# Performance work log

Measured on AMD Instinct MI355X. Metric: run time of the kernel, lower is better.

Reference implementation:

```python
import jax, jax.numpy as jnp
import numpy as np

B, E, F_DIM, D = 32, 16, 64, 512  # batch, extra dim, fea_dim, input_dim
EXP = 4                            # feed-forward expansion
EPS = 1e-5


def _layernorm(x, g, b):
    m = jnp.mean(x, axis=-1, keepdims=True)
    v = jnp.mean(jnp.square(x - m), axis=-1, keepdims=True)
    return (x - m) * jax.lax.rsqrt(v + EPS) * g + b


def setup_inputs() -> dict:
    key = jax.random.key(0)
    ks = jax.random.split(key, 12)
    s = 1.0 / np.sqrt(D)
    inp = {
        "x": jax.random.normal(ks[0], (B, E, F_DIM, D), jnp.float32),
        "ln1_g": jnp.ones((D,), jnp.float32),
        "ln1_b": jnp.zeros((D,), jnp.float32),
        "Wq": jax.random.uniform(ks[1], (D, D), jnp.float32, -s, s),
        "bq": jax.random.uniform(ks[2], (D,), jnp.float32, -s, s),
        "Wk": jax.random.uniform(ks[3], (D, D), jnp.float32, -s, s),
        "bk": jax.random.uniform(ks[4], (D,), jnp.float32, -s, s),
        "Wv": jax.random.uniform(ks[5], (D, D), jnp.float32, -s, s),
        "bv": jax.random.uniform(ks[6], (D,), jnp.float32, -s, s),
        "wn_g": jnp.ones((F_DIM,), jnp.float32),
        "wn_b": jnp.zeros((F_DIM,), jnp.float32),
        "ln2_g": jnp.ones((D,), jnp.float32),
        "ln2_b": jnp.zeros((D,), jnp.float32),
        "W1": jax.random.uniform(ks[7], (D, EXP * D), jnp.float32, -s, s),
        "b1": jax.random.uniform(ks[8], (EXP * D,), jnp.float32, -s, s),
        "W2": jax.random.uniform(ks[9], (EXP * D, D), jnp.float32, -1.0 / np.sqrt(EXP * D), 1.0 / np.sqrt(EXP * D)),
        "b2": jax.random.uniform(ks[10], (D,), jnp.float32, -1.0 / np.sqrt(EXP * D), 1.0 / np.sqrt(EXP * D)),
    }
    return inp


def reference(x, ln1_g, ln1_b, Wq, bq, Wk, bk, Wv, bv, wn_g, wn_b, ln2_g, ln2_b, W1, b1, W2, b2):
    # --- Residual 1: LN -> feature multi-head attention (dropout = identity) ---
    h = _layernorm(x, ln1_g, ln1_b)                       # [B,E,F,D]
    q = h @ Wq + bq
    k = h @ Wk + bk
    v = h @ Wv + bv
    energy = jnp.einsum('beqd,bekd->beqk', q, k)          # [B,E,F,F]
    # LayerNorm over the key axis of the raw scores (the fusion-breaking op)
    energy = _layernorm(energy, wn_g, wn_b)
    att = jax.nn.softmax(energy / jnp.sqrt(jnp.float32(D)), axis=-1)
    attn_out = jnp.einsum('beal,belv->beav', att, v)      # [B,E,F,D]
    x = x + attn_out
    # --- Residual 2: LN -> FFN (Linear -> Linear, no activation) ---
    h2 = _layernorm(x, ln2_g, ln2_b)
    ff = (h2 @ W1 + b1) @ W2 + b2
    return x + ff
```

## Files before the change

### kernel.cpp

```cpp
#include <hip/hip_runtime.h>
#include <hip/hip_bf16.h>


#define D_DIM 512
#define NROWS 32768
#define NBE   512

typedef __attribute__((ext_vector_type(8))) short bf16x8;
typedef __attribute__((ext_vector_type(4))) float f32x4;

typedef const __attribute__((address_space(1))) unsigned g_u32;
typedef __attribute__((address_space(3))) unsigned lds_u32;

__device__ __forceinline__ short f2bf(float f) {
  union { float f; unsigned u; } c; c.f = f;
  unsigned u = c.u;
  unsigned r = (u + 0x7FFFu + ((u >> 16) & 1u)) >> 16;
  return (short)r;
}
__device__ __forceinline__ float bf2f(short s) {
  union { unsigned u; float f; } c; c.u = ((unsigned)(unsigned short)s) << 16;
  return c.f;
}

__global__ __launch_bounds__(256) void wconvT(const float* __restrict__ W,
                                              short* __restrict__ Wt,
                                              int K, int N) {
  __shared__ float tile[32][33];
  const int t = threadIdx.x;
  const int r  = t >> 3;
  const int c4 = (t & 7) * 4;
  const long k0 = (long)blockIdx.y * 32;
  const long n0 = (long)blockIdx.x * 32;
  float4 v = *(const float4*)&W[(k0 + r) * N + n0 + c4];
  tile[r][c4 + 0] = v.x; tile[r][c4 + 1] = v.y;
  tile[r][c4 + 2] = v.z; tile[r][c4 + 3] = v.w;
  __syncthreads();
  union { short sh[4]; int2 v; } o;
#pragma unroll
  for (int j = 0; j < 4; ++j) o.sh[j] = f2bf(tile[c4 + j][r]);
  *(int2*)&Wt[(n0 + r) * K + k0 + c4] = o.v;
}

__global__ __launch_bounds__(256) void ln_kernel(const float* __restrict__ x,
                                                 const float* __restrict__ gam,
                                                 const float* __restrict__ bet,
                                                 short* __restrict__ h) {
  const int t = threadIdx.x;
  const long row = (long)blockIdx.x * 4 + (t >> 6);
  const int lane = t & 63;
  const float* xr = x + row * D_DIM + lane * 8;
  float4 a = *(const float4*)xr;
  float4 b = *(const float4*)(xr + 4);
  float xs[8] = {a.x, a.y, a.z, a.w, b.x, b.y, b.z, b.w};
  float s = 0.f, ss = 0.f;
#pragma unroll
  for (int j = 0; j < 8; ++j) { s += xs[j]; ss += xs[j] * xs[j]; }
#pragma unroll
  for (int m = 1; m < 64; m <<= 1) {
    s  += __shfl_xor(s, m);
    ss += __shfl_xor(ss, m);
  }
  float mean = s * (1.f / D_DIM);
  float var  = ss * (1.f / D_DIM) - mean * mean;
  float rstd = rsqrtf(var + 1e-5f);
  union { short sh[8]; int4 v; } o;
#pragma unroll
  for (int j = 0; j < 8; ++j) {
    int d = lane * 8 + j;
    o.sh[j] = f2bf((xs[j] - mean) * rstd * gam[d] + bet[d]);
  }
  *(int4*)&h[row * D_DIM + lane * 8] = o.v;
}

template <int OUT_BF16, int RESID>
__global__ __launch_bounds__(512, 2) void gemm256(
    const short* __restrict__ A, const short* __restrict__ Bt,
    const float* __restrict__ bias0, const float* __restrict__ bias1,
    const float* __restrict__ bias2,
    void* __restrict__ out0, void* __restrict__ out1, void* __restrict__ out2,
    const float* __restrict__ resid, int K, int nsplit) {
  extern __shared__ short smem[];
  short* As = smem;
  short* Bs = smem + 3 * 8192;

  const int t = threadIdx.x;
  const int wave = t >> 6, lane = t & 63;
  const int lr = lane & 15, g = lane >> 4;
  const int wr = wave >> 2, wc = wave & 3;

  const int gx = gridDim.x;
  const int nwg = gx * gridDim.y;
  const int hid = blockIdx.y * gx + blockIdx.x;
  const int lid = (hid & 7) * (nwg >> 3) + (hid >> 3);
  const int m0 = (lid / gx) * 256;
  const int n0 = (lid % gx) * 256;

  const int seg = n0 / nsplit;
  const int ncol0 = n0 - seg * nsplit;
  const float* bias = seg == 0 ? bias0 : (seg == 1 ? bias1 : bias2);
  void* outp = seg == 0 ? out0 : (seg == 1 ? out1 : out2);

  const int srow = lane & 15;
  const int scol = (lane >> 4) * 8;
  const short* gA0 = &A[(long)(m0 + wave * 32 + srow) * K + scol];
  const short* gB0 = &Bt[(long)(n0 + wave * 32 + srow) * K + scol];
  const long rstep = 16L * K;

#define STAGE_A(bufi, kk)                                                      \
  do {                                                                         \
    __builtin_amdgcn_global_load_lds((g_u32*)(gA0 + (kk)),                     \
        (lds_u32*)(As + (bufi) * 8192 + (wave * 2) * 512), 16, 0, 0);          \
    __builtin_amdgcn_global_load_lds((g_u32*)(gA0 + rstep + (kk)),             \
        (lds_u32*)(As + (bufi) * 8192 + (wave * 2 + 1) * 512), 16, 0, 0);      \
  } while (0)
#define STAGE_B(bufi, kk)                                                      \
  do {                                                                         \
    __builtin_amdgcn_global_load_lds((g_u32*)(gB0 + (kk)),                     \
        (lds_u32*)(Bs + (bufi) * 8192 + (wave * 2) * 512), 16, 0, 0);          \
    __builtin_amdgcn_global_load_lds((g_u32*)(gB0 + rstep + (kk)),             \
        (lds_u32*)(Bs + (bufi) * 8192 + (wave * 2 + 1) * 512), 16, 0, 0);      \
  } while (0)

  f32x4 acc[8][4];
  const f32x4 vzero = {0.f, 0.f, 0.f, 0.f};
#pragma unroll
  for (int mi = 0; mi < 8; ++mi)
#pragma unroll
    for (int ni = 0; ni < 4; ++ni) acc[mi][ni] = vzero;

  const int nt = K >> 5;
  STAGE_A(0, 0);  STAGE_B(0, 0);
  STAGE_A(1, 32); STAGE_B(1, 32);

  int cur = 0, stg = 2;
  const int fo = lane * 8;
  for (int T = 0; T < nt; ++T) {
    if (T < nt - 1) asm volatile("s_waitcnt vmcnt(4)" ::: "memory");
    else            asm volatile("s_waitcnt vmcnt(0)" ::: "memory");
    asm volatile("s_barrier" ::: "memory");

    if (T + 2 < nt) {
      STAGE_A(stg, (T + 2) * 32);
      STAGE_B(stg, (T + 2) * 32);
    }

    const short* sA = As + cur * 8192;
    const short* sB = Bs + cur * 8192;
    bf16x8 af[8], bfr[4];
#pragma unroll
    for (int i = 0; i < 8; ++i)
      af[i] = *(const bf16x8*)&sA[(wr * 8 + i) * 512 + fo];
#pragma unroll
    for (int i = 0; i < 4; ++i)
      bfr[i] = *(const bf16x8*)&sB[(wc * 4 + i) * 512 + fo];
#pragma unroll
    for (int mi = 0; mi < 8; ++mi)
#pragma unroll
      for (int ni = 0; ni < 4; ++ni)
        acc[mi][ni] = __builtin_amdgcn_mfma_f32_16x16x32_bf16(af[mi], bfr[ni], acc[mi][ni], 0, 0, 0);

    cur = cur == 2 ? 0 : cur + 1;
    stg = stg == 2 ? 0 : stg + 1;
  }
#undef STAGE_A
#undef STAGE_B

  __syncthreads();
  float* cs = (float*)smem + wave * 1088;
  float bv[4];
#pragma unroll
  for (int ni = 0; ni < 4; ++ni) bv[ni] = bias[ncol0 + wc * 64 + ni * 16 + lr];
  const int er = lane >> 2;
  const int ec = (lane & 3) * 16;

#pragma unroll
  for (int mi = 0; mi < 8; ++mi) {
#pragma unroll
    for (int ni = 0; ni < 4; ++ni)
#pragma unroll
      for (int r = 0; r < 4; ++r)
        cs[(g * 4 + r) * 68 + ni * 16 + lr] = acc[mi][ni][r] + bv[ni];
    const long grow = m0 + wr * 128 + mi * 16 + er;
    const long gcol = ncol0 + wc * 64 + ec;
    float vals[16];
#pragma unroll
    for (int jb = 0; jb < 4; ++jb) {
      float4 v = *(const float4*)&cs[er * 68 + ec + jb * 4];
      vals[jb * 4 + 0] = v.x; vals[jb * 4 + 1] = v.y;
      vals[jb * 4 + 2] = v.z; vals[jb * 4 + 3] = v.w;
    }
    if (RESID) {
      const float* rp = resid + grow * (long)nsplit + gcol;
#pragma unroll
      for (int jb = 0; jb < 4; ++jb) {
        float4 v = *(const float4*)&rp[jb * 4];
        vals[jb * 4 + 0] += v.x; vals[jb * 4 + 1] += v.y;
        vals[jb * 4 + 2] += v.z; vals[jb * 4 + 3] += v.w;
      }
    }
    if (OUT_BF16) {
      union { short sh[16]; int4 q[2]; } o;
#pragma unroll
      for (int j = 0; j < 16; ++j) o.sh[j] = f2bf(vals[j]);
      short* op = (short*)outp + grow * (long)nsplit + gcol;
      *(int4*)op = o.q[0];
      *(int4*)(op + 8) = o.q[1];
    } else {
      float* op = (float*)outp + grow * (long)nsplit + gcol;
#pragma unroll
      for (int jb = 0; jb < 4; ++jb)
        *(float4*)&op[jb * 4] = make_float4(vals[jb * 4 + 0], vals[jb * 4 + 1],
                                            vals[jb * 4 + 2], vals[jb * 4 + 3]);
    }
  }
}

__global__ __launch_bounds__(256) void attn_kernel(
    const short* __restrict__ q, const short* __restrict__ k,
    const short* __restrict__ v, const float* __restrict__ x,
    const float* __restrict__ wn_g, const float* __restrict__ wn_b,
    const float* __restrict__ ln2_g, const float* __restrict__ ln2_b,
    float* __restrict__ x1, short* __restrict__ h2) {
  __shared__ float att_s[64][68];
  const int t = threadIdx.x;
  const int wave = t >> 6, lane = t & 63;
  const int lr = lane & 15, g = lane >> 4;
  const long base = (long)blockIdx.x * 64;
  const long qoff = base * D_DIM;

  const f32x4 vzero = {0.f, 0.f, 0.f, 0.f};
  f32x4 acc[4];
#pragma unroll
  for (int nt = 0; nt < 4; ++nt) acc[nt] = vzero;

  for (int ks = 0; ks < 16; ++ks) {
    const int kc = ks * 32 + g * 8;
    bf16x8 afr = *(const bf16x8*)&q[qoff + (long)(wave * 16 + lr) * D_DIM + kc];
#pragma unroll
    for (int nt = 0; nt < 4; ++nt) {
      bf16x8 bfr = *(const bf16x8*)&k[qoff + (long)(nt * 16 + lr) * D_DIM + kc];
      acc[nt] = __builtin_amdgcn_mfma_f32_16x16x32_bf16(afr, bfr, acc[nt], 0, 0, 0);
    }
  }

  const float scale = 0.044194173824159216f;
#pragma unroll
  for (int r = 0; r < 4; ++r) {
    float s = 0.f, ss = 0.f;
#pragma unroll
    for (int nt = 0; nt < 4; ++nt) { float e = acc[nt][r]; s += e; ss += e * e; }
#pragma unroll
    for (int m = 1; m < 16; m <<= 1) { s += __shfl_xor(s, m); ss += __shfl_xor(ss, m); }
    float mean = s * (1.f / 64);
    float var  = ss * (1.f / 64) - mean * mean;
    float rstd = rsqrtf(var + 1e-5f);
    float e[4]; float mx = -1e30f;
#pragma unroll
    for (int nt = 0; nt < 4; ++nt) {
      int col = nt * 16 + lr;
      e[nt] = ((acc[nt][r] - mean) * rstd * wn_g[col] + wn_b[col]) * scale;
      mx = fmaxf(mx, e[nt]);
    }
#pragma unroll
    for (int m = 1; m < 16; m <<= 1) mx = fmaxf(mx, __shfl_xor(mx, m));
    float se = 0.f;
#pragma unroll
    for (int nt = 0; nt < 4; ++nt) { e[nt] = expf(e[nt] - mx); se += e[nt]; }
#pragma unroll
    for (int m = 1; m < 16; m <<= 1) se += __shfl_xor(se, m);
    float inv = 1.f / se;
#pragma unroll
    for (int nt = 0; nt < 4; ++nt)
      att_s[wave * 16 + 4 * g + r][nt * 16 + lr] = e[nt] * inv;
  }
  __syncthreads();

  const int d0 = lane * 8;
  float accp[16][8];
#pragma unroll
  for (int qi = 0; qi < 16; ++qi)
#pragma unroll
    for (int j = 0; j < 8; ++j) accp[qi][j] = 0.f;

  for (int kk0 = 0; kk0 < 64; kk0 += 4) {
    float vf[4][8];
#pragma unroll
    for (int kc = 0; kc < 4; ++kc) {
      bf16x8 vv = *(const bf16x8*)&v[qoff + (long)(kk0 + kc) * D_DIM + d0];
#pragma unroll
      for (int j = 0; j < 8; ++j) vf[kc][j] = bf2f(vv[j]);
    }
#pragma unroll
    for (int qi = 0; qi < 16; ++qi) {
      float4 a4 = *(const float4*)&att_s[wave * 16 + qi][kk0];
#pragma unroll
      for (int j = 0; j < 8; ++j) {
        accp[qi][j] += a4.x * vf[0][j];
        accp[qi][j] += a4.y * vf[1][j];
        accp[qi][j] += a4.z * vf[2][j];
        accp[qi][j] += a4.w * vf[3][j];
      }
    }
  }

  float g2v[8], b2v[8];
#pragma unroll
  for (int j = 0; j < 8; ++j) { g2v[j] = ln2_g[d0 + j]; b2v[j] = ln2_b[d0 + j]; }

#pragma unroll
  for (int qi = 0; qi < 16; ++qi) {
    const long row = base + wave * 16 + qi;
    const float* xr = x + row * D_DIM + d0;
    float4 x0 = *(const float4*)xr;
    float4 xb = *(const float4*)(xr + 4);
    accp[qi][0] += x0.x; accp[qi][1] += x0.y;
    accp[qi][2] += x0.z; accp[qi][3] += x0.w;
    accp[qi][4] += xb.x; accp[qi][5] += xb.y;
    accp[qi][6] += xb.z; accp[qi][7] += xb.w;
    float* po = x1 + row * D_DIM + d0;
    *(float4*)po       = make_float4(accp[qi][0], accp[qi][1], accp[qi][2], accp[qi][3]);
    *(float4*)(po + 4) = make_float4(accp[qi][4], accp[qi][5], accp[qi][6], accp[qi][7]);
    float s = 0.f, ss = 0.f;
#pragma unroll
    for (int j = 0; j < 8; ++j) { s += accp[qi][j]; ss += accp[qi][j] * accp[qi][j]; }
#pragma unroll
    for (int m = 1; m < 64; m <<= 1) { s += __shfl_xor(s, m); ss += __shfl_xor(ss, m); }
    float mean = s * (1.f / D_DIM);
    float var  = ss * (1.f / D_DIM) - mean * mean;
    float rstd = rsqrtf(var + 1e-5f);
    union { short sh[8]; int4 v; } o;
#pragma unroll
    for (int j = 0; j < 8; ++j)
      o.sh[j] = f2bf((accp[qi][j] - mean) * rstd * g2v[j] + b2v[j]);
    *(int4*)&h2[row * D_DIM + d0] = o.v;
  }
}

extern "C" void kernel_launch(void* const* d_in, const int* in_sizes, int n_in,
                              void* d_out, int out_size, void* d_ws, size_t ws_size,
                              hipStream_t stream) {
  (void)in_sizes; (void)n_in; (void)out_size; (void)ws_size;
  const float* x     = (const float*)d_in[0];
  const float* ln1_g = (const float*)d_in[1];
  const float* ln1_b = (const float*)d_in[2];
  const float* Wq    = (const float*)d_in[3];
  const float* bq    = (const float*)d_in[4];
  const float* Wk    = (const float*)d_in[5];
  const float* bk    = (const float*)d_in[6];
  const float* Wv    = (const float*)d_in[7];
  const float* bv    = (const float*)d_in[8];
  const float* wn_g  = (const float*)d_in[9];
  const float* wn_b  = (const float*)d_in[10];
  const float* ln2_g = (const float*)d_in[11];
  const float* ln2_b = (const float*)d_in[12];
  const float* W1    = (const float*)d_in[13];
  const float* b1    = (const float*)d_in[14];
  const float* W2    = (const float*)d_in[15];
  const float* b2    = (const float*)d_in[16];
  float* out = (float*)d_out;

  char* ws = (char*)d_ws;
  short* h   = (short*)(ws);
  short* qb  = (short*)(ws + (size_t)32  * 1024 * 1024);
  short* kb  = (short*)(ws + (size_t)64  * 1024 * 1024);
  short* vb  = (short*)(ws + (size_t)96  * 1024 * 1024);
  short* ff1 = (short*)(ws + (size_t)32  * 1024 * 1024);
  short* Wqt = (short*)(ws + (size_t)160 * 1024 * 1024);
  short* Wkt = Wqt + 512 * 512;
  short* Wvt = Wkt + 512 * 512;
  short* W1t = Wvt + 512 * 512;
  short* W2t = W1t + 512 * 2048;

  const size_t lds_bytes = 3 * 8192 * 2 * 2;
  (void)hipFuncSetAttribute((const void*)gemm256<1, 0>,
      hipFuncAttributeMaxDynamicSharedMemorySize, (int)lds_bytes);
  (void)hipFuncSetAttribute((const void*)gemm256<0, 1>,
      hipFuncAttributeMaxDynamicSharedMemorySize, (int)lds_bytes);

  wconvT<<<dim3(512 / 32, 512 / 32),  256, 0, stream>>>(Wq, Wqt, 512, 512);
  wconvT<<<dim3(512 / 32, 512 / 32),  256, 0, stream>>>(Wk, Wkt, 512, 512);
  wconvT<<<dim3(512 / 32, 512 / 32),  256, 0, stream>>>(Wv, Wvt, 512, 512);
  wconvT<<<dim3(2048 / 32, 512 / 32), 256, 0, stream>>>(W1, W1t, 512, 2048);
  wconvT<<<dim3(512 / 32, 2048 / 32), 256, 0, stream>>>(W2, W2t, 2048, 512);

  ln_kernel<<<NROWS / 4, 256, 0, stream>>>(x, ln1_g, ln1_b, h);

  dim3 gqkv(1536 / 256, NROWS / 256);
  gemm256<1, 0><<<gqkv, 512, lds_bytes, stream>>>(h, Wqt, bq, bk, bv,
                                                  qb, kb, vb, nullptr, 512, 512);

  attn_kernel<<<NBE, 256, 0, stream>>>(qb, kb, vb, x, wn_g, wn_b,
                                       ln2_g, ln2_b, out, h);

  dim3 gff1(2048 / 256, NROWS / 256);
  gemm256<1, 0><<<gff1, 512, lds_bytes, stream>>>(h, W1t, b1, b1, b1,
                                                  ff1, ff1, ff1, nullptr, 512, 2048);

  dim3 gff2(512 / 256, NROWS / 256);
  gemm256<0, 1><<<gff2, 512, lds_bytes, stream>>>(ff1, W2t, b2, b2, b2,
                                                  out, out, out, out, 2048, 512);
}
```

Measured before the change: 507.8 us.

## Restructure GEMM to double-buffered BK=64 with XOR-swizzled row-major LDS tiles

The 256x256 GEMM's K-step grows from 32 to 64 and staging moves from a triple-buffered, fragment-ordered LDS layout to a double-buffered row-major layout with an XOR swizzle that avoids bank conflicts. Each iteration now issues 16 MFMAs per fragment set across two K halves and uses a __syncthreads per step, replacing the manual vmcnt waits and s_barrier. LDS rises to 128 KB and the min-blocks-per-CU hint of 2 is removed, which halves barriers per unit of K but lowers occupancy. Prefetch depth drops from two stages ahead to one.

```diff
diff --git a/kernel.cpp b/kernel.cpp
--- a/kernel.cpp
+++ b/kernel.cpp
@@ -74,7 +74,7 @@
 }
 
 template <int OUT_BF16, int RESID>
-__global__ __launch_bounds__(512, 2) void gemm256(
+__global__ __launch_bounds__(512) void gemm256(
     const short* __restrict__ A, const short* __restrict__ Bt,
     const float* __restrict__ bias0, const float* __restrict__ bias1,
     const float* __restrict__ bias2,
@@ -82,7 +82,7 @@
     const float* __restrict__ resid, int K, int nsplit) {
   extern __shared__ short smem[];
   short* As = smem;
-  short* Bs = smem + 3 * 8192;
+  short* Bs = smem + 2 * 16384;
 
   const int t = threadIdx.x;
   const int wave = t >> 6, lane = t & 63;
@@ -101,25 +101,23 @@
   const float* bias = seg == 0 ? bias0 : (seg == 1 ? bias1 : bias2);
   void* outp = seg == 0 ? out0 : (seg == 1 ? out1 : out2);
 
-  const int srow = lane & 15;
-  const int scol = (lane >> 4) * 8;
-  const short* gA0 = &A[(long)(m0 + wave * 32 + srow) * K + scol];
-  const short* gB0 = &Bt[(long)(n0 + wave * 32 + srow) * K + scol];
-  const long rstep = 16L * K;
-
-#define STAGE_A(bufi, kk)                                                      \
+  const int srow = lane >> 3;
+  const int skel = 8 * ((lane & 7) ^ srow);
+  const short* gA0 = &A[(long)(m0 + wave * 32 + srow) * K + skel];
+  const short* gB0 = &Bt[(long)(n0 + wave * 32 + srow) * K + skel];
+  const long rstep8 = 8L * K;
+
+#define STAGE(bufi, kk)                                                        \
   do {                                                                         \
-    __builtin_amdgcn_global_load_lds((g_u32*)(gA0 + (kk)),                     \
-        (lds_u32*)(As + (bufi) * 8192 + (wave * 2) * 512), 16, 0, 0);          \
-    __builtin_amdgcn_global_load_lds((g_u32*)(gA0 + rstep + (kk)),             \
-        (lds_u32*)(As + (bufi) * 8192 + (wave * 2 + 1) * 512), 16, 0, 0);      \
-  } while (0)
-#define STAGE_B(bufi, kk)                                                      \
-  do {                                                                         \
-    __builtin_amdgcn_global_load_lds((g_u32*)(gB0 + (kk)),                     \
-        (lds_u32*)(Bs + (bufi) * 8192 + (wave * 2) * 512), 16, 0, 0);          \
-    __builtin_amdgcn_global_load_lds((g_u32*)(gB0 + rstep + (kk)),             \
-        (lds_u32*)(Bs + (bufi) * 8192 + (wave * 2 + 1) * 512), 16, 0, 0);      \
+    _Pragma("unroll")                                                          \
+    for (int i = 0; i < 4; ++i) {                                              \
+      __builtin_amdgcn_global_load_lds((g_u32*)(gA0 + i * rstep8 + (kk)),      \
+          (lds_u32*)(As + (bufi) * 16384 + wave * 2048 + i * 512 + lane * 8),  \
+          16, 0, 0);                                                           \
+      __builtin_amdgcn_global_load_lds((g_u32*)(gB0 + i * rstep8 + (kk)),      \
+          (lds_u32*)(Bs + (bufi) * 16384 + wave * 2048 + i * 512 + lane * 8),  \
+          16, 0, 0);                                                           \
+    }                                                                          \
   } while (0)
 
   f32x4 acc[8][4];
@@ -129,44 +127,44 @@
 #pragma unroll
     for (int ni = 0; ni < 4; ++ni) acc[mi][ni] = vzero;
 
-  const int nt = K >> 5;
-  STAGE_A(0, 0);  STAGE_B(0, 0);
-  STAGE_A(1, 32); STAGE_B(1, 32);
-
-  int cur = 0, stg = 2;
-  const int fo = lane * 8;
+  const int nt = K >> 6;
+  STAGE(0, 0);
+  __syncthreads();
+
+  const int fswz = (lr & 7) * 8;
+  int cur = 0;
   for (int T = 0; T < nt; ++T) {
-    if (T < nt - 1) asm volatile("s_waitcnt vmcnt(4)" ::: "memory");
-    else            asm volatile("s_waitcnt vmcnt(0)" ::: "memory");
-    asm volatile("s_barrier" ::: "memory");
-
-    if (T + 2 < nt) {
-      STAGE_A(stg, (T + 2) * 32);
-      STAGE_B(stg, (T + 2) * 32);
-    }
-
-    const short* sA = As + cur * 8192;
-    const short* sB = Bs + cur * 8192;
-    bf16x8 af[8], bfr[4];
-#pragma unroll
-    for (int i = 0; i < 8; ++i)
-      af[i] = *(const bf16x8*)&sA[(wr * 8 + i) * 512 + fo];
-#pragma unroll
-    for (int i = 0; i < 4; ++i)
-      bfr[i] = *(const bf16x8*)&sB[(wc * 4 + i) * 512 + fo];
-#pragma unroll
-    for (int mi = 0; mi < 8; ++mi)
-#pragma unroll
-      for (int ni = 0; ni < 4; ++ni)
-        acc[mi][ni] = __builtin_amdgcn_mfma_f32_16x16x32_bf16(af[mi], bfr[ni], acc[mi][ni], 0, 0, 0);
-
-    cur = cur == 2 ? 0 : cur + 1;
-    stg = stg == 2 ? 0 : stg + 1;
-  }
-#undef STAGE_A
-#undef STAGE_B
-
-  __syncthreads();
+    if (T + 1 < nt) STAGE(cur ^ 1, (T + 1) * 64);
+    const short* sA = As + cur * 16384;
+    const short* sB = Bs + cur * 16384;
+    bf16x8 af[8][2], bfr[4][2];
+#pragma unroll
+    for (int c = 0; c < 8; ++c) {
+      const int rbase = (wr * 128 + c * 16 + lr) * 64;
+#pragma unroll
+      for (int t2 = 0; t2 < 2; ++t2)
+        af[c][t2] = *(const bf16x8*)&sA[rbase + ((t2 * 32 + g * 8) ^ fswz)];
+    }
+#pragma unroll
+    for (int c = 0; c < 4; ++c) {
+      const int rbase = (wc * 64 + c * 16 + lr) * 64;
+#pragma unroll
+      for (int t2 = 0; t2 < 2; ++t2)
+        bfr[c][t2] = *(const bf16x8*)&sB[rbase + ((t2 * 32 + g * 8) ^ fswz)];
+    }
+#pragma unroll
+    for (int t2 = 0; t2 < 2; ++t2)
+#pragma unroll
+      for (int mi = 0; mi < 8; ++mi)
+#pragma unroll
+        for (int ni = 0; ni < 4; ++ni)
+          acc[mi][ni] = __builtin_amdgcn_mfma_f32_16x16x32_bf16(
+              af[mi][t2], bfr[ni][t2], acc[mi][ni], 0, 0, 0);
+    __syncthreads();
+    cur ^= 1;
+  }
+#undef STAGE
+
   float* cs = (float*)smem + wave * 1088;
   float bv[4];
 #pragma unroll
@@ -372,7 +370,7 @@
   short* W1t = Wvt + 512 * 512;
   short* W2t = W1t + 512 * 2048;
 
-  const size_t lds_bytes = 3 * 8192 * 2 * 2;
+  const size_t lds_bytes = 4 * 16384 * 2;
   (void)hipFuncSetAttribute((const void*)gemm256<1, 0>,
       hipFuncAttributeMaxDynamicSharedMemorySize, (int)lds_bytes);
   (void)hipFuncSetAttribute((const void*)gemm256<0, 1>,
```

Result: faster. 496.4 us (-2.3%).

## Restructure GEMM main loop into 4-phase ping-pong schedule with 64-wide K tiles

Applied to the files above, without the earlier changes.

Rewrites the gemm256 main loop to use 64-wide K tiles split into two 32-wide halves, double-buffered in 128 KB of LDS. Each iteration runs four phases, each loading a fragment set, issuing one quarter of the next tiles' global-to-LDS loads, and then doing MFMAs at raised wave priority between barriers. The aim is to interleave memory traffic with matrix work and reduce stall time at barriers. In exchange the larger LDS footprint drops occupancy to one workgroup per CU (launch bounds changed to match), and the schedule adds many more barriers.

```diff
diff --git a/kernel.cpp b/kernel.cpp
--- a/kernel.cpp
+++ b/kernel.cpp
@@ -74,16 +74,13 @@
 }
 
 template <int OUT_BF16, int RESID>
-__global__ __launch_bounds__(512, 2) void gemm256(
+__global__ __launch_bounds__(512) void gemm256(
     const short* __restrict__ A, const short* __restrict__ Bt,
     const float* __restrict__ bias0, const float* __restrict__ bias1,
     const float* __restrict__ bias2,
     void* __restrict__ out0, void* __restrict__ out1, void* __restrict__ out2,
     const float* __restrict__ resid, int K, int nsplit) {
   extern __shared__ short smem[];
-  short* As = smem;
-  short* Bs = smem + 3 * 8192;
-
   const int t = threadIdx.x;
   const int wave = t >> 6, lane = t & 63;
   const int lr = lane & 15, g = lane >> 4;
@@ -101,25 +98,27 @@
   const float* bias = seg == 0 ? bias0 : (seg == 1 ? bias1 : bias2);
   void* outp = seg == 0 ? out0 : (seg == 1 ? out1 : out2);
 
-  const int srow = lane & 15;
-  const int scol = (lane >> 4) * 8;
-  const short* gA0 = &A[(long)(m0 + wave * 32 + srow) * K + scol];
-  const short* gB0 = &Bt[(long)(n0 + wave * 32 + srow) * K + scol];
-  const long rstep = 16L * K;
-
-#define STAGE_A(bufi, kk)                                                      \
+  const short* gA0 = &A[(long)(m0 + wave * 16 + lr) * K + g * 8];
+  const short* gB0 = &Bt[(long)(n0 + wave * 16 + lr) * K + g * 8];
+  const long rstep = 128L * K;
+  const int ldst = wave * 512 + lane * 8;
+
+#define STG_A(bb, kh, Ti)                                                      \
   do {                                                                         \
-    __builtin_amdgcn_global_load_lds((g_u32*)(gA0 + (kk)),                     \
-        (lds_u32*)(As + (bufi) * 8192 + (wave * 2) * 512), 16, 0, 0);          \
-    __builtin_amdgcn_global_load_lds((g_u32*)(gA0 + rstep + (kk)),             \
-        (lds_u32*)(As + (bufi) * 8192 + (wave * 2 + 1) * 512), 16, 0, 0);      \
+    const long gk = (long)(Ti) * 64 + (kh) * 32;                               \
+    __builtin_amdgcn_global_load_lds((g_u32*)(gA0 + gk),                       \
+        (lds_u32*)(smem + ((bb) * 2 + (kh)) * 8192 + ldst), 16, 0, 0);         \
+    __builtin_amdgcn_global_load_lds((g_u32*)(gA0 + rstep + gk),               \
+        (lds_u32*)(smem + ((bb) * 2 + (kh)) * 8192 + 4096 + ldst), 16, 0, 0);  \
   } while (0)
-#define STAGE_B(bufi, kk)                                                      \
+#define STG_B(bb, kh, Ti)                                                      \
   do {                                                                         \
-    __builtin_amdgcn_global_load_lds((g_u32*)(gB0 + (kk)),                     \
-        (lds_u32*)(Bs + (bufi) * 8192 + (wave * 2) * 512), 16, 0, 0);          \
-    __builtin_amdgcn_global_load_lds((g_u32*)(gB0 + rstep + (kk)),             \
-        (lds_u32*)(Bs + (bufi) * 8192 + (wave * 2 + 1) * 512), 16, 0, 0);      \
+    const long gk = (long)(Ti) * 64 + (kh) * 32;                               \
+    __builtin_amdgcn_global_load_lds((g_u32*)(gB0 + gk),                       \
+        (lds_u32*)(smem + 32768 + ((bb) * 2 + (kh)) * 8192 + ldst), 16, 0, 0); \
+    __builtin_amdgcn_global_load_lds((g_u32*)(gB0 + rstep + gk),               \
+        (lds_u32*)(smem + 32768 + ((bb) * 2 + (kh)) * 8192 + 4096 + ldst),     \
+        16, 0, 0);                                                             \
   } while (0)
 
   f32x4 acc[8][4];
@@ -129,44 +128,92 @@
 #pragma unroll
     for (int ni = 0; ni < 4; ++ni) acc[mi][ni] = vzero;
 
-  const int nt = K >> 5;
-  STAGE_A(0, 0);  STAGE_B(0, 0);
-  STAGE_A(1, 32); STAGE_B(1, 32);
-
-  int cur = 0, stg = 2;
+  const int nt = K >> 6;
+  STG_A(0, 0, 0); STG_B(0, 0, 0);
+  STG_A(0, 1, 0); STG_B(0, 1, 0);
+  STG_A(1, 0, 1); STG_B(1, 0, 1);
+  asm volatile("s_waitcnt vmcnt(4)" ::: "memory");
+  __builtin_amdgcn_s_barrier();
+
   const int fo = lane * 8;
   for (int T = 0; T < nt; ++T) {
-    if (T < nt - 1) asm volatile("s_waitcnt vmcnt(4)" ::: "memory");
-    else            asm volatile("s_waitcnt vmcnt(0)" ::: "memory");
-    asm volatile("s_barrier" ::: "memory");
-
-    if (T + 2 < nt) {
-      STAGE_A(stg, (T + 2) * 32);
-      STAGE_B(stg, (T + 2) * 32);
-    }
-
-    const short* sA = As + cur * 8192;
-    const short* sB = Bs + cur * 8192;
-    bf16x8 af[8], bfr[4];
-#pragma unroll
-    for (int i = 0; i < 8; ++i)
-      af[i] = *(const bf16x8*)&sA[(wr * 8 + i) * 512 + fo];
-#pragma unroll
-    for (int i = 0; i < 4; ++i)
-      bfr[i] = *(const bf16x8*)&sB[(wc * 4 + i) * 512 + fo];
-#pragma unroll
-    for (int mi = 0; mi < 8; ++mi)
+    const int bb = T & 1, nb = bb ^ 1;
+    const short* sA0 = smem + (bb * 2 + 0) * 8192;
+    const short* sA1 = smem + (bb * 2 + 1) * 8192;
+    const short* sB0 = smem + 32768 + (bb * 2 + 0) * 8192;
+    const short* sB1 = smem + 32768 + (bb * 2 + 1) * 8192;
+    bf16x8 af[4], bfr[4];
+
+#pragma unroll
+    for (int i = 0; i < 4; ++i) af[i]  = *(const bf16x8*)&sA0[(wr * 8 + i) * 512 + fo];
+#pragma unroll
+    for (int i = 0; i < 4; ++i) bfr[i] = *(const bf16x8*)&sB0[(wc * 4 + i) * 512 + fo];
+    if (T + 1 < nt) STG_A(nb, 1, T + 1);
+    __builtin_amdgcn_s_barrier();
+    asm volatile("s_waitcnt lgkmcnt(0)" ::: "memory");
+    __builtin_amdgcn_sched_barrier(0);
+    __builtin_amdgcn_s_setprio(1);
+#pragma unroll
+    for (int mi = 0; mi < 4; ++mi)
 #pragma unroll
       for (int ni = 0; ni < 4; ++ni)
         acc[mi][ni] = __builtin_amdgcn_mfma_f32_16x16x32_bf16(af[mi], bfr[ni], acc[mi][ni], 0, 0, 0);
-
-    cur = cur == 2 ? 0 : cur + 1;
-    stg = stg == 2 ? 0 : stg + 1;
-  }
-#undef STAGE_A
-#undef STAGE_B
-
-  __syncthreads();
+    __builtin_amdgcn_s_setprio(0);
+    __builtin_amdgcn_s_barrier();
+
+#pragma unroll
+    for (int i = 0; i < 4; ++i) af[i] = *(const bf16x8*)&sA0[(wr * 8 + 4 + i) * 512 + fo];
+    if (T + 1 < nt) STG_B(nb, 1, T + 1);
+    __builtin_amdgcn_s_barrier();
+    asm volatile("s_waitcnt lgkmcnt(0)" ::: "memory");
+    __builtin_amdgcn_sched_barrier(0);
+    __builtin_amdgcn_s_setprio(1);
+#pragma unroll
+    for (int mi = 0; mi < 4; ++mi)
+#pragma unroll
+      for (int ni = 0; ni < 4; ++ni)
+        acc[4 + mi][ni] = __builtin_amdgcn_mfma_f32_16x16x32_bf16(af[mi], bfr[ni], acc[4 + mi][ni], 0, 0, 0);
+    __builtin_amdgcn_s_setprio(0);
+    __builtin_amdgcn_s_barrier();
+
+#pragma unroll
+    for (int i = 0; i < 4; ++i) af[i]  = *(const bf16x8*)&sA1[(wr * 8 + i) * 512 + fo];
+#pragma unroll
+    for (int i = 0; i < 4; ++i) bfr[i] = *(const bf16x8*)&sB1[(wc * 4 + i) * 512 + fo];
+    if (T + 2 < nt) STG_A(bb, 0, T + 2);
+    __builtin_amdgcn_s_barrier();
+    asm volatile("s_waitcnt lgkmcnt(0)" ::: "memory");
+    __builtin_amdgcn_sched_barrier(0);
+    __builtin_amdgcn_s_setprio(1);
+#pragma unroll
+    for (int mi = 0; mi < 4; ++mi)
+#pragma unroll
+      for (int ni = 0; ni < 4; ++ni)
+        acc[mi][ni] = __builtin_amdgcn_mfma_f32_16x16x32_bf16(af[mi], bfr[ni], acc[mi][ni], 0, 0, 0);
+    __builtin_amdgcn_s_setprio(0);
+    __builtin_amdgcn_s_barrier();
+
+#pragma unroll
+    for (int i = 0; i < 4; ++i) af[i] = *(const bf16x8*)&sA1[(wr * 8 + 4 + i) * 512 + fo];
+    if (T + 2 < nt) STG_B(bb, 0, T + 2);
+    __builtin_amdgcn_s_barrier();
+    asm volatile("s_waitcnt lgkmcnt(0)" ::: "memory");
+    __builtin_amdgcn_sched_barrier(0);
+    __builtin_amdgcn_s_setprio(1);
+#pragma unroll
+    for (int mi = 0; mi < 4; ++mi)
+#pragma unroll
+      for (int ni = 0; ni < 4; ++ni)
+        acc[4 + mi][ni] = __builtin_amdgcn_mfma_f32_16x16x32_bf16(af[mi], bfr[ni], acc[4 + mi][ni], 0, 0, 0);
+    __builtin_amdgcn_s_setprio(0);
+
+    if (T + 2 < nt) asm volatile("s_waitcnt vmcnt(4)" ::: "memory");
+    else            asm volatile("s_waitcnt vmcnt(0)" ::: "memory");
+    __builtin_amdgcn_s_barrier();
+  }
+#undef STG_A
+#undef STG_B
+
   float* cs = (float*)smem + wave * 1088;
   float bv[4];
 #pragma unroll
@@ -372,7 +419,7 @@
   short* W1t = Wvt + 512 * 512;
   short* W2t = W1t + 512 * 2048;
 
-  const size_t lds_bytes = 3 * 8192 * 2 * 2;
+  const size_t lds_bytes = 131072;
   (void)hipFuncSetAttribute((const void*)gemm256<1, 0>,
       hipFuncAttributeMaxDynamicSharedMemorySize, (int)lds_bytes);
   (void)hipFuncSetAttribute((const void*)gemm256<0, 1>,
```

Result: slower. 521.1 us (+2.6%).
